# Kernel tuning notes

Measured on AMD Instinct MI355X. Metric: run time of the kernel, lower is better.

The kernel has to match this reference:

```python
import jax, jax.numpy as jnp
import numpy as np

STATE_SIZE = 29
ACTION_SIZE = 3


def setup_inputs() -> dict:
    key = jax.random.key(0)
    ks = jax.random.split(key, 12)

    def row_norm(k, shape, scale=1.0):
        w = jax.random.normal(k, shape, dtype=jnp.float32)
        return w * (scale / jnp.sqrt(jnp.sum(w * w, axis=1, keepdims=True)))

    lrelu_gain = float(np.sqrt(2.0 / (1.0 + 0.01 ** 2)))  # torch calculate_gain('leaky_relu')
    inp = {
        "x": jax.random.normal(ks[0], (1, STATE_SIZE), dtype=jnp.float32),
        "hx": jnp.zeros((1, 128), jnp.float32),
        "cx": jnp.zeros((1, 128), jnp.float32),
        "w1": row_norm(ks[1], (256, STATE_SIZE)) * lrelu_gain,
        "b1": jnp.zeros((256,), jnp.float32),
        "w2": row_norm(ks[2], (256, 256)) * lrelu_gain,
        "b2": jnp.zeros((256,), jnp.float32),
        "w3": row_norm(ks[3], (128, 256)) * lrelu_gain,
        "b3": jnp.zeros((128,), jnp.float32),
        "w4": row_norm(ks[4], (128, 128)) * lrelu_gain,
        "b4": jnp.zeros((128,), jnp.float32),
        "w_ih": jax.random.normal(ks[5], (512, 128), dtype=jnp.float32) * 0.08,
        "b_ih": jnp.zeros((512,), jnp.float32),
        "w_hh": jax.random.normal(ks[6], (512, 128), dtype=jnp.float32) * 0.08,
        "b_hh": jnp.zeros((512,), jnp.float32),
        "w_critic": row_norm(ks[7], (1, 128), 1.0),
        "b_critic": jnp.zeros((1,), jnp.float32),
        "w_actor": row_norm(ks[8], (ACTION_SIZE, 128), 0.01),
        "b_actor": jnp.zeros((ACTION_SIZE,), jnp.float32),
        "w_actor2": row_norm(ks[9], (ACTION_SIZE, 128), 0.01),
        "b_actor2": jnp.zeros((ACTION_SIZE,), jnp.float32),
    }
    return inp


def _lrelu(v):
    return jnp.where(v > 0, v, 0.1 * v)


def reference(x, hx, cx, w1, b1, w2, b2, w3, b3, w4, b4,
              w_ih, b_ih, w_hh, b_hh,
              w_critic, b_critic, w_actor, b_actor, w_actor2, b_actor2):
    h = _lrelu(x @ w1.T + b1)
    h = _lrelu(h @ w2.T + b2)
    h = _lrelu(h @ w3.T + b3)
    h = _lrelu(h @ w4.T + b4)            # [1,128]
    # LSTMCell: gate order i, f, g, o (PyTorch convention)
    gates = h @ w_ih.T + b_ih + hx @ w_hh.T + b_hh  # [1,512]
    i, f, g, o = jnp.split(gates, 4, axis=-1)
    c_new = jax.nn.sigmoid(f) * cx + jax.nn.sigmoid(i) * jnp.tanh(g)
    h_new = jax.nn.sigmoid(o) * jnp.tanh(c_new)      # [1,128]
    value = jnp.squeeze(h_new @ w_critic.T + b_critic)          # scalar
    actor = jax.nn.soft_sign(h_new @ w_actor.T + b_actor)
    actor = jnp.squeeze(actor)                                   # [action_size]
    actor2 = jnp.squeeze(h_new @ w_actor2.T + b_actor2)         # [action_size]
    return (value, actor, actor2)
```

## Files before the change

kernel.cpp:

```cpp
#include <hip/hip_runtime.h>
#include <math.h>


#define NB   32
#define TPB  256
#define MAGIC 0x3A3C5A17u

#define H2_OFF 0
#define H3_OFF 256
#define H4_OFF 384
#define PT_OFF 512

__device__ __forceinline__ float lrelu(float v) { return v > 0.f ? v : 0.1f * v; }
__device__ __forceinline__ float sigm(float v)  { return 1.f / (1.f + __expf(-v)); }
__device__ __forceinline__ float dot4(float4 a, float4 b) {
    return a.x * b.x + a.y * b.y + a.z * b.z + a.w * b.w;
}

__device__ __forceinline__ void send(unsigned long long* p, float v) {
    unsigned lo = __float_as_uint(v);
    unsigned long long pk = (unsigned long long)lo |
                            ((unsigned long long)(lo ^ MAGIC) << 32);
    __hip_atomic_store(p, pk, __ATOMIC_RELAXED, __HIP_MEMORY_SCOPE_AGENT);
}
__device__ __forceinline__ float recv(unsigned long long* p) {
    unsigned long long pk =
        __hip_atomic_load(p, __ATOMIC_RELAXED, __HIP_MEMORY_SCOPE_AGENT);
    unsigned lo = (unsigned)pk, hi = (unsigned)(pk >> 32);
    if ((lo ^ MAGIC) == hi) return __uint_as_float(lo);
    __builtin_amdgcn_s_sleep(2);
    for (;;) {
        pk = __hip_atomic_load(p, __ATOMIC_RELAXED, __HIP_MEMORY_SCOPE_AGENT);
        lo = (unsigned)pk; hi = (unsigned)(pk >> 32);
        if ((lo ^ MAGIC) == hi) return __uint_as_float(lo);
        __builtin_amdgcn_s_sleep(8);
    }
}
__device__ __forceinline__ void touch(unsigned long long* p) {
    unsigned long long v =
        __hip_atomic_load(p, __ATOMIC_RELAXED, __HIP_MEMORY_SCOPE_AGENT);
    asm volatile("" :: "v"(v));
}

__global__ __launch_bounds__(TPB, 1) void a3c_fwd(
    const float* __restrict__ x, const float* __restrict__ hx, const float* __restrict__ cx,
    const float* __restrict__ w1, const float* __restrict__ b1,
    const float* __restrict__ w2, const float* __restrict__ b2,
    const float* __restrict__ w3, const float* __restrict__ b3,
    const float* __restrict__ w4, const float* __restrict__ b4,
    const float* __restrict__ w_ih, const float* __restrict__ b_ih,
    const float* __restrict__ w_hh, const float* __restrict__ b_hh,
    const float* __restrict__ w_critic, const float* __restrict__ b_critic,
    const float* __restrict__ w_actor, const float* __restrict__ b_actor,
    const float* __restrict__ w_actor2, const float* __restrict__ b_actor2,
    float* __restrict__ out, unsigned long long* __restrict__ wsp)
{
    const int blk = blockIdx.x, tid = threadIdx.x;

    if (blk < 16) {
        const int b = blk;
        if (tid == 0) touch(wsp + H2_OFF + b * 16);
        if (tid == 1) touch(wsp + H2_OFF + b * 16 + 8);

        float a1[29];
        {
            const float* w1r = w1 + tid * 29;
            #pragma unroll
            for (int j = 0; j < 29; ++j) a1[j] = w1r[j];
        }
        const float bb1 = b1[tid];

        const int r2 = b * 16 + (tid >> 4), p2 = tid & 15;
        float4 a2[4];
        {
            const float4* wp = (const float4*)(w2 + r2 * 256 + p2 * 16);
            #pragma unroll
            for (int j = 0; j < 4; ++j) a2[j] = wp[j];
        }
        const float bb2 = b2[r2];

        __shared__ __align__(16) float x_s[32];
        __shared__ __align__(16) float h1_s[256];
        if (tid < 32) x_s[tid] = (tid < 29) ? x[tid] : 0.f;
        __syncthreads();

        {
            float s = 0.f;
            #pragma unroll
            for (int j = 0; j < 29; ++j) s += a1[j] * x_s[j];
            h1_s[tid] = lrelu(s + bb1);
        }
        __syncthreads();

        {
            const float4* hp = (const float4*)(h1_s + p2 * 16);
            float s = 0.f;
            #pragma unroll
            for (int j = 0; j < 4; ++j) s += dot4(a2[j], hp[j]);
            s += __shfl_xor(s, 1); s += __shfl_xor(s, 2);
            s += __shfl_xor(s, 4); s += __shfl_xor(s, 8);
            if (p2 == 0) send(wsp + H2_OFF + r2, lrelu(s + bb2));
        }
        return;
    }

    if (blk < 20) {
        const int c = blk - 16;
        if (tid < 16)       touch(wsp + H2_OFF + tid * 16);
        else if (tid < 20)  touch(wsp + H3_OFF + c * 32 + (tid - 16) * 8);

        const int r3 = c * 32 + (tid >> 3), p3 = tid & 7;
        float4 a3[8];
        {
            const float4* wp = (const float4*)(w3 + r3 * 256 + p3 * 32);
            #pragma unroll
            for (int j = 0; j < 8; ++j) a3[j] = wp[j];
        }
        const float bb3 = b3[r3];

        __shared__ __align__(16) float h2_s[256];
        h2_s[tid] = recv(wsp + H2_OFF + tid);
        __syncthreads();

        const float4* hp = (const float4*)(h2_s + p3 * 32);
        float s = 0.f;
        #pragma unroll
        for (int j = 0; j < 8; ++j) s += dot4(a3[j], hp[j]);
        s += __shfl_xor(s, 1); s += __shfl_xor(s, 2); s += __shfl_xor(s, 4);
        if (p3 == 0) send(wsp + H3_OFF + r3, lrelu(s + bb3));
        return;
    }

    if (blk < 24) {
        const int d = blk - 20;
        if (tid < 8)        touch(wsp + H3_OFF + tid * 16);
        else if (tid < 12)  touch(wsp + H4_OFF + d * 32 + (tid - 8) * 8);

        const int r4 = d * 32 + (tid >> 3), p4 = tid & 7;
        float4 a4[4];
        {
            const float4* wp = (const float4*)(w4 + r4 * 128 + p4 * 16);
            #pragma unroll
            for (int j = 0; j < 4; ++j) a4[j] = wp[j];
        }
        const float bb4 = b4[r4];

        __shared__ __align__(16) float h3_s[128];
        if (tid < 128) h3_s[tid] = recv(wsp + H3_OFF + tid);
        __syncthreads();

        const float4* hp = (const float4*)(h3_s + p4 * 16);
        float s = 0.f;
        #pragma unroll
        for (int j = 0; j < 4; ++j) s += dot4(a4[j], hp[j]);
        s += __shfl_xor(s, 1); s += __shfl_xor(s, 2); s += __shfl_xor(s, 4);
        if (p4 == 0) send(wsp + H4_OFF + r4, lrelu(s + bb4));
        return;
    }

    {
        const int g = blk - 24;
        if (tid < 8) touch(wsp + H4_OFF + tid * 16);
        if (g > 0) { if (tid == 8) touch(wsp + PT_OFF + g * 8); }
        else       { if (tid >= 9 && tid < 16) touch(wsp + PT_OFF + (tid - 8) * 8); }

        const int r = tid >> 2, p = tid & 3;
        const int gate = r >> 4, cell = r & 15;
        const int grow = gate * 128 + g * 16 + cell;

        float4 ah[8];
        {
            const float4* wp = (const float4*)(w_hh + grow * 128 + p * 32);
            #pragma unroll
            for (int j = 0; j < 8; ++j) ah[j] = wp[j];
        }
        float4 ai[8];
        {
            const float4* wp = (const float4*)(w_ih + grow * 128 + p * 32);
            #pragma unroll
            for (int j = 0; j < 8; ++j) ai[j] = wp[j];
        }
        const float bsum = b_ih[grow] + b_hh[grow];

        __shared__ __align__(16) float hx_s[128];
        __shared__ __align__(16) float h4_s[128];
        __shared__ __align__(16) float g_s[64];
        __shared__ __align__(16) float hn_s[16];
        __shared__ __align__(16) float hw_s[112];
        __shared__ __align__(16) float hb_s[8];
        __shared__ __align__(16) float ps[56];

        if (tid < 128) hx_s[tid] = hx[tid];
        float cxv = (tid < 16) ? cx[g * 16 + tid] : 0.f;
        if (tid < 112) {
            int o = tid >> 4, c = tid & 15;
            float v;
            if (o == 0)      v = w_critic[g * 16 + c];
            else if (o < 4)  v = w_actor [(o - 1) * 128 + g * 16 + c];
            else             v = w_actor2[(o - 4) * 128 + g * 16 + c];
            hw_s[tid] = v;
        }
        if (g == 0 && tid == 0) {
            hb_s[0] = b_critic[0];
            hb_s[1] = b_actor[0];  hb_s[2] = b_actor[1];  hb_s[3] = b_actor[2];
            hb_s[4] = b_actor2[0]; hb_s[5] = b_actor2[1]; hb_s[6] = b_actor2[2];
        }
        __syncthreads();

        float g0;
        {
            const float4* hp = (const float4*)(hx_s + p * 32);
            float s = 0.f;
            #pragma unroll
            for (int j = 0; j < 8; ++j) s += dot4(ah[j], hp[j]);
            s += __shfl_xor(s, 1); s += __shfl_xor(s, 2);
            g0 = s + bsum;
        }

        if (tid < 128) h4_s[tid] = recv(wsp + H4_OFF + tid);
        __syncthreads();

        {
            const float4* hp = (const float4*)(h4_s + p * 32);
            float s = 0.f;
            #pragma unroll
            for (int j = 0; j < 8; ++j) s += dot4(ai[j], hp[j]);
            s += __shfl_xor(s, 1); s += __shfl_xor(s, 2);
            if (p == 0) g_s[r] = g0 + s;
        }
        __syncthreads();

        if (tid < 16) {
            float ig = g_s[tid];
            float fg = g_s[16 + tid];
            float gg = g_s[32 + tid];
            float og = g_s[48 + tid];
            float c  = sigm(fg) * cxv + sigm(ig) * tanhf(gg);
            hn_s[tid] = sigm(og) * tanhf(c);
        }
        __syncthreads();

        if (tid < 7) {
            const float* wc = hw_s + tid * 16;
            float s = 0.f;
            #pragma unroll
            for (int j = 0; j < 16; ++j) s += wc[j] * hn_s[j];
            if (g > 0) send(wsp + PT_OFF + g * 8 + tid, s);
            else       ps[tid * 8] = s + hb_s[tid];
        }

        if (g == 0) {
            if (tid < 56) {
                const int gg = (tid >> 3) + 1, h = tid & 7;
                if (h < 7) ps[h * 8 + gg] = recv(wsp + PT_OFF + gg * 8 + h);
            }
            __syncthreads();
            if (tid < 7) {
                const float* row = ps + tid * 8;
                float s = row[0] + row[1] + row[2] + row[3]
                        + row[4] + row[5] + row[6] + row[7];
                if (tid >= 1 && tid <= 3) s = s / (1.f + fabsf(s));
                out[tid] = s;
            }
        }
    }
}

extern "C" void kernel_launch(void* const* d_in, const int* in_sizes, int n_in,
                              void* d_out, int out_size, void* d_ws, size_t ws_size,
                              hipStream_t stream) {
    const float* x        = (const float*)d_in[0];
    const float* hx       = (const float*)d_in[1];
    const float* cx       = (const float*)d_in[2];
    const float* w1       = (const float*)d_in[3];
    const float* b1       = (const float*)d_in[4];
    const float* w2       = (const float*)d_in[5];
    const float* b2       = (const float*)d_in[6];
    const float* w3       = (const float*)d_in[7];
    const float* b3       = (const float*)d_in[8];
    const float* w4       = (const float*)d_in[9];
    const float* b4       = (const float*)d_in[10];
    const float* w_ih     = (const float*)d_in[11];
    const float* b_ih     = (const float*)d_in[12];
    const float* w_hh     = (const float*)d_in[13];
    const float* b_hh     = (const float*)d_in[14];
    const float* w_critic = (const float*)d_in[15];
    const float* b_critic = (const float*)d_in[16];
    const float* w_actor  = (const float*)d_in[17];
    const float* b_actor  = (const float*)d_in[18];
    const float* w_actor2 = (const float*)d_in[19];
    const float* b_actor2 = (const float*)d_in[20];
    float* out = (float*)d_out;
    unsigned long long* wsp = (unsigned long long*)d_ws;

    a3c_fwd<<<NB, TPB, 0, stream>>>(x, hx, cx, w1, b1, w2, b2, w3, b3, w4, b4,
                                    w_ih, b_ih, w_hh, b_hh,
                                    w_critic, b_critic, w_actor, b_actor,
                                    w_actor2, b_actor2, out, wsp);
}
```

Baseline: 100.7 us.

## Fold layer-4 into LSTM blocks and halve layer-2 block count

Reduces the grid from 32 to 20 blocks. Layer-2 now uses 8 blocks with 32 rows each instead of 16 blocks with 16 rows. Layer-4 no longer has its own 4 blocks: each of the 8 LSTM blocks computes its 16 rows of h4 from h3, keeps its own slice locally and receives the other slices through the flag-packed workspace. This removes one full inter-block stage hop. In exchange, the LSTM blocks carry extra weight loads and an added all-to-all exchange among themselves.

Measured after the change: 104.5 us. +3.7%, slower.

```diff
diff --git a/kernel.cpp b/kernel.cpp
--- a/kernel.cpp
+++ b/kernel.cpp
@@ -2,7 +2,7 @@
 #include <math.h>
 
 
-#define NB   32
+#define NB   20
 #define TPB  256
 #define MAGIC 0x3A3C5A17u
 
@@ -57,10 +57,9 @@
 {
     const int blk = blockIdx.x, tid = threadIdx.x;
 
-    if (blk < 16) {
+    if (blk < 8) {
         const int b = blk;
-        if (tid == 0) touch(wsp + H2_OFF + b * 16);
-        if (tid == 1) touch(wsp + H2_OFF + b * 16 + 8);
+        if (tid < 4) touch(wsp + H2_OFF + b * 32 + tid * 8);
 
         float a1[29];
         {
@@ -70,12 +69,12 @@
         }
         const float bb1 = b1[tid];
 
-        const int r2 = b * 16 + (tid >> 4), p2 = tid & 15;
-        float4 a2[4];
-        {
-            const float4* wp = (const float4*)(w2 + r2 * 256 + p2 * 16);
-            #pragma unroll
-            for (int j = 0; j < 4; ++j) a2[j] = wp[j];
+        const int r2 = b * 32 + (tid >> 3), p2 = tid & 7;
+        float4 a2[8];
+        {
+            const float4* wp = (const float4*)(w2 + r2 * 256 + p2 * 32);
+            #pragma unroll
+            for (int j = 0; j < 8; ++j) a2[j] = wp[j];
         }
         const float bb2 = b2[r2];
 
@@ -93,19 +92,18 @@
         __syncthreads();
 
         {
-            const float4* hp = (const float4*)(h1_s + p2 * 16);
-            float s = 0.f;
-            #pragma unroll
-            for (int j = 0; j < 4; ++j) s += dot4(a2[j], hp[j]);
-            s += __shfl_xor(s, 1); s += __shfl_xor(s, 2);
-            s += __shfl_xor(s, 4); s += __shfl_xor(s, 8);
+            const float4* hp = (const float4*)(h1_s + p2 * 32);
+            float s = 0.f;
+            #pragma unroll
+            for (int j = 0; j < 8; ++j) s += dot4(a2[j], hp[j]);
+            s += __shfl_xor(s, 1); s += __shfl_xor(s, 2); s += __shfl_xor(s, 4);
             if (p2 == 0) send(wsp + H2_OFF + r2, lrelu(s + bb2));
         }
         return;
     }
 
-    if (blk < 20) {
-        const int c = blk - 16;
+    if (blk < 12) {
+        const int c = blk - 8;
         if (tid < 16)       touch(wsp + H2_OFF + tid * 16);
         else if (tid < 20)  touch(wsp + H3_OFF + c * 32 + (tid - 16) * 8);
 
@@ -131,42 +129,19 @@
         return;
     }
 
-    if (blk < 24) {
-        const int d = blk - 20;
-        if (tid < 8)        touch(wsp + H3_OFF + tid * 16);
-        else if (tid < 12)  touch(wsp + H4_OFF + d * 32 + (tid - 8) * 8);
-
-        const int r4 = d * 32 + (tid >> 3), p4 = tid & 7;
-        float4 a4[4];
-        {
-            const float4* wp = (const float4*)(w4 + r4 * 128 + p4 * 16);
-            #pragma unroll
-            for (int j = 0; j < 4; ++j) a4[j] = wp[j];
-        }
-        const float bb4 = b4[r4];
-
-        __shared__ __align__(16) float h3_s[128];
-        if (tid < 128) h3_s[tid] = recv(wsp + H3_OFF + tid);
-        __syncthreads();
-
-        const float4* hp = (const float4*)(h3_s + p4 * 16);
-        float s = 0.f;
-        #pragma unroll
-        for (int j = 0; j < 4; ++j) s += dot4(a4[j], hp[j]);
-        s += __shfl_xor(s, 1); s += __shfl_xor(s, 2); s += __shfl_xor(s, 4);
-        if (p4 == 0) send(wsp + H4_OFF + r4, lrelu(s + bb4));
-        return;
-    }
-
     {
-        const int g = blk - 24;
-        if (tid < 8) touch(wsp + H4_OFF + tid * 16);
-        if (g > 0) { if (tid == 8) touch(wsp + PT_OFF + g * 8); }
-        else       { if (tid >= 9 && tid < 16) touch(wsp + PT_OFF + (tid - 8) * 8); }
+        const int g = blk - 12;
+        if (tid < 8)                 touch(wsp + H3_OFF + tid * 16);
+        else if (tid == 8)           touch(wsp + H4_OFF + g * 16);
+        else if (tid == 9)           touch(wsp + H4_OFF + g * 16 + 8);
+        else if (g > 0 && tid == 10) touch(wsp + PT_OFF + g * 8);
+        else if (g == 0 && tid >= 10 && tid < 18)
+                                     touch(wsp + PT_OFF + (tid - 10) * 8);
 
         const int r = tid >> 2, p = tid & 3;
         const int gate = r >> 4, cell = r & 15;
         const int grow = gate * 128 + g * 16 + cell;
+        const int rl4 = tid >> 4, p4 = tid & 15;
 
         float4 ah[8];
         {
@@ -174,6 +149,11 @@
             #pragma unroll
             for (int j = 0; j < 8; ++j) ah[j] = wp[j];
         }
+        float4 a4v0, a4v1;
+        {
+            const float4* wp = (const float4*)(w4 + (g * 16 + rl4) * 128 + p4 * 8);
+            a4v0 = wp[0]; a4v1 = wp[1];
+        }
         float4 ai[8];
         {
             const float4* wp = (const float4*)(w_ih + grow * 128 + p * 32);
@@ -181,14 +161,16 @@
             for (int j = 0; j < 8; ++j) ai[j] = wp[j];
         }
         const float bsum = b_ih[grow] + b_hh[grow];
+        const float bb4  = b4[g * 16 + rl4];
 
         __shared__ __align__(16) float hx_s[128];
+        __shared__ __align__(16) float h3_s[128];
         __shared__ __align__(16) float h4_s[128];
         __shared__ __align__(16) float g_s[64];
         __shared__ __align__(16) float hn_s[16];
         __shared__ __align__(16) float hw_s[112];
         __shared__ __align__(16) float hb_s[8];
-        __shared__ __align__(16) float ps[56];
+        __shared__ __align__(16) float ps[64];
 
         if (tid < 128) hx_s[tid] = hx[tid];
         float cxv = (tid < 16) ? cx[g * 16 + tid] : 0.f;
@@ -217,7 +199,21 @@
             g0 = s + bsum;
         }
 
-        if (tid < 128) h4_s[tid] = recv(wsp + H4_OFF + tid);
+        if (tid < 128) h3_s[tid] = recv(wsp + H3_OFF + tid);
+        __syncthreads();
+
+        {
+            const float4* hp = (const float4*)(h3_s + p4 * 8);
+            float s = dot4(a4v0, hp[0]) + dot4(a4v1, hp[1]);
+            s += __shfl_xor(s, 1); s += __shfl_xor(s, 2);
+            s += __shfl_xor(s, 4); s += __shfl_xor(s, 8);
+            if (p4 == 0) {
+                float v = lrelu(s + bb4);
+                h4_s[g * 16 + rl4] = v;
+                send(wsp + H4_OFF + g * 16 + rl4, v);
+            }
+        }
+        if (tid < 128 && (tid >> 4) != g) h4_s[tid] = recv(wsp + H4_OFF + tid);
         __syncthreads();
 
         {
```

## Split layer-1 across blocks and exchange activations through global flags

Applied to the files above, without the earlier changes.

Previously every one of the 16 layer-2 blocks computed all 256 layer-1 outputs redundantly, with each thread loading 29 strided weights. Now each block computes only its own 16 rows of layer 1, using a 16-lane shuffle reduction. It publishes those rows through tagged atomic stores in the workspace and spin-receives the remaining 240 values from the other blocks. This removes redundant weight loads and arithmetic, but adds a cross-block dependency and a global-memory round trip before layer 2 can start.

After: 103.3 us. 1.03x slower.

```diff
diff --git a/kernel.cpp b/kernel.cpp
--- a/kernel.cpp
+++ b/kernel.cpp
@@ -6,10 +6,11 @@
 #define TPB  256
 #define MAGIC 0x3A3C5A17u
 
-#define H2_OFF 0
-#define H3_OFF 256
-#define H4_OFF 384
-#define PT_OFF 512
+#define H1_OFF 0
+#define H2_OFF 256
+#define H3_OFF 512
+#define H4_OFF 640
+#define PT_OFF 768
 
 __device__ __forceinline__ float lrelu(float v) { return v > 0.f ? v : 0.1f * v; }
 __device__ __forceinline__ float sigm(float v)  { return 1.f / (1.f + __expf(-v)); }
@@ -59,18 +60,17 @@
 
     if (blk < 16) {
         const int b = blk;
-        if (tid == 0) touch(wsp + H2_OFF + b * 16);
-        if (tid == 1) touch(wsp + H2_OFF + b * 16 + 8);
-
-        float a1[29];
-        {
-            const float* w1r = w1 + tid * 29;
-            #pragma unroll
-            for (int j = 0; j < 29; ++j) a1[j] = w1r[j];
-        }
-        const float bb1 = b1[tid];
-
-        const int r2 = b * 16 + (tid >> 4), p2 = tid & 15;
+        if (tid < 16)      touch(wsp + H1_OFF + tid * 16);
+        else if (tid < 18) touch(wsp + H2_OFF + b * 16 + (tid - 16) * 8);
+
+        const int r1 = b * 16 + (tid >> 4), p1 = tid & 15;
+        const int c0 = p1 * 2;
+        float a1x = 0.f, a1y = 0.f;
+        if (c0 < 29)     a1x = w1[r1 * 29 + c0];
+        if (c0 + 1 < 29) a1y = w1[r1 * 29 + c0 + 1];
+        const float bb1 = b1[r1];
+
+        const int r2 = r1, p2 = p1;
         float4 a2[4];
         {
             const float4* wp = (const float4*)(w2 + r2 * 256 + p2 * 16);
@@ -85,11 +85,16 @@
         __syncthreads();
 
         {
-            float s = 0.f;
-            #pragma unroll
-            for (int j = 0; j < 29; ++j) s += a1[j] * x_s[j];
-            h1_s[tid] = lrelu(s + bb1);
-        }
+            float s = a1x * x_s[c0] + a1y * x_s[c0 + 1];
+            s += __shfl_xor(s, 1); s += __shfl_xor(s, 2);
+            s += __shfl_xor(s, 4); s += __shfl_xor(s, 8);
+            if (p1 == 0) {
+                float v = lrelu(s + bb1);
+                h1_s[r1] = v;
+                send(wsp + H1_OFF + r1, v);
+            }
+        }
+        if ((tid >> 4) != b) h1_s[tid] = recv(wsp + H1_OFF + tid);
         __syncthreads();
 
         {
@@ -188,7 +193,7 @@
         __shared__ __align__(16) float hn_s[16];
         __shared__ __align__(16) float hw_s[112];
         __shared__ __align__(16) float hb_s[8];
-        __shared__ __align__(16) float ps[56];
+        __shared__ __align__(16) float ps[64];
 
         if (tid < 128) hx_s[tid] = hx[tid];
         float cxv = (tid < 16) ? cx[g * 16 + tid] : 0.f;
```
